# Kernel optimization log

Hardware: AMD Instinct MI355X
Metric: run time of the kernel (lower is better)

The kernel has to match this reference:

```python
import jax, jax.numpy as jnp
import numpy as np

DT_MIN, DT_MAX = 1e-3, 1e-1
LN_EPS = 1e-5


def layernorm(x, w, b):
    mu = jnp.mean(x, axis=-1, keepdims=True)
    var = jnp.mean(jnp.square(x - mu), axis=-1, keepdims=True)
    return (x - mu) * jax.lax.rsqrt(var + LN_EPS) * w + b


def _scan(Lam_bar, Bu, reverse=False):
    # Lam_bar: (P,) complex64; Bu: (B, L, P) complex64
    A = jnp.broadcast_to(Lam_bar, Bu.shape)

    def binop(e_i, e_j):
        a_i, b_i = e_i
        a_j, b_j = e_j
        return a_j * a_i, a_j * b_i + b_j

    _, xs = jax.lax.associative_scan(binop, (A, Bu), axis=1, reverse=reverse)
    return xs  # (B, L, P)


def s5_ssm(u, Lambda_re, Lambda_im, log_step, B_re, B_im, C_re, C_im, D):
    # u: (B, L, H) real. Diagonal S5 with ZOH discretization, bidirectional.
    step = jnp.exp(log_step)                          # (P,)
    Lam = (Lambda_re + 1j * Lambda_im).astype(jnp.complex64)
    Lam_bar = jnp.exp(Lam * step)                     # (P,)
    Bmat = (B_re + 1j * B_im).astype(jnp.complex64)   # (P, H)
    B_bar = ((Lam_bar - 1.0) / Lam)[:, None] * Bmat   # (P, H)
    Bu = jnp.einsum('blh,ph->blp', u.astype(jnp.complex64), B_bar)  # (B,L,P)
    xs_f = _scan(Lam_bar, Bu, reverse=False)
    xs_b = _scan(Lam_bar, Bu, reverse=True)
    xs = jnp.concatenate([xs_f, xs_b], axis=-1)       # (B, L, 2P)
    C = (C_re + 1j * C_im).astype(jnp.complex64)      # (H, 2P)
    ys = 2.0 * jnp.einsum('hp,blp->blh', C, xs).real  # conj-symmetric output
    return ys + D * u


def gelu(x):
    return jax.nn.gelu(x, approximate=False)  # torch default (erf) gelu


def s5_block(x, ln1_w, ln1_b, ln2_w, ln2_b, Lambda_re, Lambda_im, log_step,
             B_re, B_im, C_re, C_im, D, ff_enc_w, ff_dec_w):
    # attention-style half: pre-LN + S5 + gelu + residual (residual = normed input)
    fx = layernorm(x, ln1_w, ln1_b)
    res = fx
    x = gelu(s5_ssm(fx, Lambda_re, Lambda_im, log_step, B_re, B_im, C_re, C_im, D)) + res
    # FFN half: pre-LN + GEGLU + residual (residual = normed input)
    fx = layernorm(x, ln2_w, ln2_b)
    res = fx
    h = fx @ ff_enc_w.T                               # (B, L, 2*dim)
    a, g = jnp.split(h, 2, axis=-1)
    x = (a * gelu(g)) @ ff_dec_w.T + res
    return x


def setup_inputs() -> dict:
    B, L, D_IN, DIM, P = 4, 4096, 512, 1024, 512
    key = jax.random.key(0)
    ks = jax.random.split(key, 16)
    inp = {}
    inp['x'] = jax.random.normal(ks[0], (B, L, D_IN), dtype=jnp.float32)
    inp['W_in'] = jax.random.normal(ks[1], (DIM, D_IN), jnp.float32) / np.sqrt(D_IN)
    inp['W_out'] = jax.random.normal(ks[2], (D_IN, DIM), jnp.float32) / np.sqrt(DIM)
    inp['ln1_w'] = jnp.ones((DIM,), jnp.float32)
    inp['ln1_b'] = jnp.zeros((DIM,), jnp.float32)
    inp['ln2_w'] = jnp.ones((DIM,), jnp.float32)
    inp['ln2_b'] = jnp.zeros((DIM,), jnp.float32)
    inp['Lambda_re'] = -0.5 * jnp.exp(jax.random.normal(ks[3], (P,), jnp.float32))
    inp['Lambda_im'] = jnp.pi * jax.random.normal(ks[4], (P,), jnp.float32)
    inp['log_step'] = jax.random.uniform(ks[5], (P,), jnp.float32,
                                         minval=np.log(DT_MIN), maxval=np.log(DT_MAX))
    inp['B_re'] = jax.random.normal(ks[6], (P, DIM), jnp.float32) / np.sqrt(DIM)
    inp['B_im'] = jax.random.normal(ks[7], (P, DIM), jnp.float32) / np.sqrt(DIM)
    inp['C_re'] = jax.random.normal(ks[8], (DIM, 2 * P), jnp.float32) / np.sqrt(2 * P)
    inp['C_im'] = jax.random.normal(ks[9], (DIM, 2 * P), jnp.float32) / np.sqrt(2 * P)
    inp['D'] = jax.random.normal(ks[10], (DIM,), jnp.float32)
    inp['ff_enc_w'] = jax.random.normal(ks[11], (2 * DIM, DIM), jnp.float32) / np.sqrt(DIM)
    inp['ff_dec_w'] = jax.random.normal(ks[12], (DIM, DIM), jnp.float32) / np.sqrt(DIM)
    return inp


def reference(x, W_in, W_out, ln1_w, ln1_b, ln2_w, ln2_b, Lambda_re, Lambda_im,
              log_step, B_re, B_im, C_re, C_im, D, ff_enc_w, ff_dec_w):
    h = x @ W_in.T                                    # (B, L, dim)
    h = s5_block(h, ln1_w, ln1_b, ln2_w, ln2_b, Lambda_re, Lambda_im, log_step,
                 B_re, B_im, C_re, C_im, D, ff_enc_w, ff_dec_w)
    return h @ W_out.T                                # (B, L, d_input)
```

## Files before the change

kernel.cpp:

```cpp
#include <hip/hip_runtime.h>
#include <cstdint>

typedef __bf16 bf16;
typedef __bf16 bf16x2 __attribute__((ext_vector_type(2)));
typedef __bf16 bf16x4 __attribute__((ext_vector_type(4)));
typedef __bf16 bf16x8 __attribute__((ext_vector_type(8)));
typedef float f32x4 __attribute__((ext_vector_type(4)));

#define MROWS 16384
#define DIMH 1024
#define PDIM 512
#define LSEQ 4096
#define CL 16
#define NC (LSEQ / CL)

typedef const __attribute__((address_space(1))) unsigned int* gas_t;
typedef __attribute__((address_space(3))) unsigned int* las_t;

__device__ __forceinline__ float gelu_f(float x) {
  return 0.5f * x * (1.0f + erff(x * 0.70710678118654752f));
}

__global__ void k_prep(const float* __restrict__ Lre, const float* __restrict__ Lim,
                       const float* __restrict__ lstep,
                       float2* __restrict__ lamb, float2* __restrict__ coef) {
  const int p = blockIdx.x * blockDim.x + threadIdx.x;
  if (p >= PDIM) return;
  const float lre = Lre[p], lim = Lim[p];
  const float st = expf(lstep[p]);
  const float er = expf(lre * st);
  const float lbr = er * cosf(lim * st);
  const float lbi = er * sinf(lim * st);
  lamb[p] = make_float2(lbr, lbi);
  const float ar = lbr - 1.0f, ai = lbi;
  const float d = lre * lre + lim * lim;
  coef[p] = make_float2((ar * lre + ai * lim) / d, (ai * lre - ar * lim) / d);
}

__global__ void k_f32_to_bf16(const float* __restrict__ in, bf16* __restrict__ outp, int n) {
  const int i = (blockIdx.x * 256 + threadIdx.x) * 4;
  if (i >= n) return;
  const float4 v = *(const float4*)(in + i);
  bf16x4 o = { (bf16)v.x, (bf16)v.y, (bf16)v.z, (bf16)v.w };
  *(bf16x4*)(outp + i) = o;
}

__global__ void k_bcat(const float* __restrict__ Bre, const float* __restrict__ Bim,
                       const float2* __restrict__ coef, bf16* __restrict__ bcat) {
  const int idx = blockIdx.x * 256 + threadIdx.x;
  const int p = idx >> 10;
  const float2 c = coef[p];
  const float br = Bre[idx], bi = Bim[idx];
  bcat[idx] = (bf16)(c.x * br - c.y * bi);
  bcat[idx + PDIM * DIMH] = (bf16)(c.x * bi + c.y * br);
}

__global__ void k_ccomb(const float* __restrict__ Cre, const float* __restrict__ Cim,
                        bf16* __restrict__ cc) {
  const int idx = blockIdx.x * 256 + threadIdx.x;
  const int n = idx >> 11, k = idx & 2047;
  float v;
  if (k < 512)       v =  2.0f * Cre[n * 1024 + k];
  else if (k < 1024) v = -2.0f * Cim[n * 1024 + (k - 512)];
  else if (k < 1536) v =  2.0f * Cre[n * 1024 + 512 + (k - 1024)];
  else               v = -2.0f * Cim[n * 1024 + 512 + (k - 1536)];
  cc[idx] = (bf16)v;
}


#define VMCNT4 asm volatile("s_waitcnt vmcnt(4)" ::: "memory")
#define VMCNT0 asm volatile("s_waitcnt vmcnt(0)" ::: "memory")
#define LGKM0  asm volatile("s_waitcnt lgkmcnt(0)" ::: "memory")
#define SCHED0 __builtin_amdgcn_sched_barrier(0)
#define BAR    __builtin_amdgcn_s_barrier()

#define PHASE(slot, kh, mh, LOADB, STAGE_STMT, WAIT_STMT)                      \
  {                                                                            \
    if (LOADB) ldB(slot, kh, bfr);                                             \
    ldA(slot, kh, mh, afr);                                                    \
    STAGE_STMT;                                                                \
    SCHED0;                                                                    \
    BAR;                                                                       \
    LGKM0;                                                                     \
    SCHED0;                                                                    \
    __builtin_amdgcn_s_setprio(1);                                             \
    _Pragma("unroll")                                                          \
    for (int m = 0; m < 4; ++m)                                                \
      _Pragma("unroll")                                                        \
      for (int n = 0; n < 4; ++n)                                              \
        acc[(mh) * 4 + m][n] = __builtin_amdgcn_mfma_f32_16x16x32_bf16(        \
            afr[m], bfr[n], acc[(mh) * 4 + m][n], 0, 0, 0);                    \
    __builtin_amdgcn_s_setprio(0);                                             \
    SCHED0;                                                                    \
    WAIT_STMT;                                                                 \
    BAR;                                                                       \
  }

template <int EPI>
__global__ __launch_bounds__(512, 2) void k_gemm(const bf16* __restrict__ A,
                                                 const bf16* __restrict__ W,
                                                 float* __restrict__ Cf,
                                                 bf16* __restrict__ Cb,
                                                 const bf16* __restrict__ auxb,
                                                 int K, int N, int nbnl) {
  extern __shared__ char lds[];
  const int q = (int)gridDim.x >> 3;
  const int s = ((int)blockIdx.x & 7) * q + ((int)blockIdx.x >> 3);
  const int bm = s >> nbnl;
  const int bn = s & ((1 << nbnl) - 1);
  const int tid = threadIdx.x;
  const int lane = tid & 63;
  const int wave = tid >> 6;
  const int wr = wave >> 2;
  const int wc = wave & 3;

  const size_t arow0 = (size_t)bm * 256;
  const size_t wrow0 = (size_t)bn * 256;
  const int srow = tid >> 2;
  const int schunk = (tid & 3) ^ ((tid >> 3) & 3);
  const int wbase = wave << 10;

  f32x4 acc[8][4];
#pragma unroll
  for (int i = 0; i < 8; ++i)
#pragma unroll
    for (int j = 0; j < 4; ++j) acc[i][j] = (f32x4){0.f, 0.f, 0.f, 0.f};

  auto stage = [&](int slot, int kh, int kt) {
    const int kcol = kt * 64 + kh * 32 + schunk * 8;
    {
      char* base = lds + slot * 32768 + kh * 16384;
      __builtin_amdgcn_global_load_lds(
          (gas_t)(A + (arow0 + srow) * (size_t)K + kcol), (las_t)(base + wbase), 16, 0, 0);
      __builtin_amdgcn_global_load_lds(
          (gas_t)(A + (arow0 + 128 + srow) * (size_t)K + kcol), (las_t)(base + 8192 + wbase), 16, 0, 0);
    }
    {
      char* base = lds + 65536 + slot * 32768 + kh * 16384;
      __builtin_amdgcn_global_load_lds(
          (gas_t)(W + (wrow0 + srow) * (size_t)K + kcol), (las_t)(base + wbase), 16, 0, 0);
      __builtin_amdgcn_global_load_lds(
          (gas_t)(W + (wrow0 + 128 + srow) * (size_t)K + kcol), (las_t)(base + 8192 + wbase), 16, 0, 0);
    }
  };

  auto ldA = [&](int slot, int kh, int mh, bf16x8* af) {
#pragma unroll
    for (int m = 0; m < 4; ++m) {
      const int row = wr * 128 + mh * 64 + m * 16 + (lane & 15);
      const int pc = (lane >> 4) ^ ((row >> 1) & 3);
      af[m] = *(const bf16x8*)(lds + slot * 32768 + kh * 16384 + row * 64 + pc * 16);
    }
  };
  auto ldB = [&](int slot, int kh, bf16x8* bf) {
#pragma unroll
    for (int n = 0; n < 4; ++n) {
      const int row = wc * 64 + n * 16 + (lane & 15);
      const int pc = (lane >> 4) ^ ((row >> 1) & 3);
      bf[n] = *(const bf16x8*)(lds + 65536 + slot * 32768 + kh * 16384 + row * 64 + pc * 16);
    }
  };

  bf16x8 afr[4], bfr[4];

  stage(0, 0, 0);
  stage(0, 1, 0);
  stage(1, 0, 1);
  VMCNT4;
  BAR;

  const int NT = K >> 7;
  for (int t = 0; t < NT; ++t) {
    const int nl = (t + 1 < NT);
    PHASE(0, 0, 0, 1, stage(1, 1, 2 * t + 1), (void)0);
    PHASE(0, 0, 1, 0, (void)0, (void)0);
    PHASE(0, 1, 0, 1, if (nl) stage(0, 0, 2 * t + 2), (void)0);
    if (nl) { PHASE(0, 1, 1, 0, (void)0, VMCNT4); }
    else    { PHASE(0, 1, 1, 0, (void)0, VMCNT0); }
    PHASE(1, 0, 0, 1, if (nl) stage(0, 1, 2 * t + 2), (void)0);
    PHASE(1, 0, 1, 0, (void)0, (void)0);
    PHASE(1, 1, 0, 1, if (nl) stage(1, 0, 2 * t + 3), (void)0);
    if (nl) { PHASE(1, 1, 1, 0, (void)0, VMCNT4); }
    else    { PHASE(1, 1, 1, 0, (void)0, (void)0); }
  }

  const int n0 = (int)wrow0 + wc * 64 + (lane & 15);
  const size_t m0 = arow0 + wr * 128 + ((lane >> 4) << 2);
#pragma unroll
  for (int mi = 0; mi < 8; ++mi)
#pragma unroll
    for (int n = 0; n < 4; ++n) {
      const size_t mb = m0 + mi * 16;
      const int nn = n0 + n * 16;
#pragma unroll
      for (int r = 0; r < 4; ++r) {
        const size_t idx = (mb + r) * (size_t)N + nn;
        const float v = acc[mi][n][r];
        if constexpr (EPI == 0) {
          Cf[idx] = v;
        } else if constexpr (EPI == 1) {
          Cb[idx] = (bf16)((float)auxb[idx] * gelu_f(v));
        } else if constexpr (EPI == 2) {
          Cb[idx] = (bf16)(v + (float)auxb[idx]);
        } else {
          Cb[idx] = (bf16)v;
        }
      }
    }
}

__global__ __launch_bounds__(256) void k_ln(const bf16* __restrict__ X,
                                            const float* __restrict__ w,
                                            const float* __restrict__ bb,
                                            bf16* __restrict__ Yb) {
  const int m = blockIdx.x;
  const int tid = threadIdx.x;
  const bf16x4 v4 = *(const bf16x4*)(X + (size_t)m * DIMH + tid * 4);
  const float v0 = (float)v4[0], v1 = (float)v4[1], v2 = (float)v4[2], v3 = (float)v4[3];
  float s = v0 + v1 + v2 + v3;
  float s2 = v0 * v0 + v1 * v1 + v2 * v2 + v3 * v3;
#pragma unroll
  for (int off = 32; off > 0; off >>= 1) { s += __shfl_down(s, off); s2 += __shfl_down(s2, off); }
  __shared__ float rs[4], rq[4];
  if ((tid & 63) == 0) { rs[tid >> 6] = s; rq[tid >> 6] = s2; }
  __syncthreads();
  s = rs[0] + rs[1] + rs[2] + rs[3];
  s2 = rq[0] + rq[1] + rq[2] + rq[3];
  const float mu = s * (1.0f / DIMH);
  const float inv = rsqrtf(s2 * (1.0f / DIMH) - mu * mu + 1e-5f);
  const float4 wv = ((const float4*)w)[tid];
  const float4 bv = ((const float4*)bb)[tid];
  bf16x4 ob = { (bf16)((v0 - mu) * inv * wv.x + bv.x), (bf16)((v1 - mu) * inv * wv.y + bv.y),
                (bf16)((v2 - mu) * inv * wv.z + bv.z), (bf16)((v3 - mu) * inv * wv.w + bv.w) };
  *(bf16x4*)(Yb + (size_t)m * DIMH + tid * 4) = ob;
}

__global__ __launch_bounds__(256) void k_ln2e(const bf16* __restrict__ YS,
                                              bf16* FXE,
                                              const float* __restrict__ Dv,
                                              const float* __restrict__ w,
                                              const float* __restrict__ bb) {
  const int m = blockIdx.x;
  const int tid = threadIdx.x;
  const bf16x4 ys4 = *(const bf16x4*)(YS + (size_t)m * DIMH + tid * 4);
  const bf16x4 fx4 = *(const bf16x4*)(FXE + (size_t)m * DIMH + tid * 4);
  const float4 dv = ((const float4*)Dv)[tid];
  const float f0 = (float)fx4[0], f1 = (float)fx4[1], f2 = (float)fx4[2], f3 = (float)fx4[3];
  const float t0 = gelu_f((float)ys4[0] + dv.x * f0) + f0;
  const float t1 = gelu_f((float)ys4[1] + dv.y * f1) + f1;
  const float t2 = gelu_f((float)ys4[2] + dv.z * f2) + f2;
  const float t3 = gelu_f((float)ys4[3] + dv.w * f3) + f3;
  float s = t0 + t1 + t2 + t3;
  float s2 = t0 * t0 + t1 * t1 + t2 * t2 + t3 * t3;
#pragma unroll
  for (int off = 32; off > 0; off >>= 1) { s += __shfl_down(s, off); s2 += __shfl_down(s2, off); }
  __shared__ float rs[4], rq[4];
  if ((tid & 63) == 0) { rs[tid >> 6] = s; rq[tid >> 6] = s2; }
  __syncthreads();
  s = rs[0] + rs[1] + rs[2] + rs[3];
  s2 = rq[0] + rq[1] + rq[2] + rq[3];
  const float mu = s * (1.0f / DIMH);
  const float inv = rsqrtf(s2 * (1.0f / DIMH) - mu * mu + 1e-5f);
  const float4 wv = ((const float4*)w)[tid];
  const float4 bv = ((const float4*)bb)[tid];
  bf16x4 ob = { (bf16)((t0 - mu) * inv * wv.x + bv.x), (bf16)((t1 - mu) * inv * wv.y + bv.y),
                (bf16)((t2 - mu) * inv * wv.z + bv.z), (bf16)((t3 - mu) * inv * wv.w + bv.w) };
  *(bf16x4*)(FXE + (size_t)m * DIMH + tid * 4) = ob;
}

__global__ __launch_bounds__(256) void k_scanA(const bf16* __restrict__ Bu,
                                               const float2* __restrict__ lamb,
                                               float2* __restrict__ carry) {
  const int bc = blockIdx.x;
  const int b = bc >> 8, c = bc & (NC - 1);
  const int t = threadIdx.x;
  const size_t rbase = ((size_t)b * LSEQ + (size_t)c * CL) * DIMH;
  float2 re[CL], im[CL];
#pragma unroll
  for (int i = 0; i < CL; ++i) {
    const bf16x2 r2 = *(const bf16x2*)(Bu + rbase + (size_t)i * DIMH + 2 * t);
    const bf16x2 i2 = *(const bf16x2*)(Bu + rbase + (size_t)i * DIMH + PDIM + 2 * t);
    re[i] = make_float2((float)r2[0], (float)r2[1]);
    im[i] = make_float2((float)i2[0], (float)i2[1]);
  }
  const float2 l0 = lamb[2 * t];
  const float2 l1 = lamb[2 * t + 1];
  const size_t cb = ((size_t)bc * 2) * PDIM;
  {
    float s0r = 0.f, s0i = 0.f, s1r = 0.f, s1i = 0.f;
#pragma unroll
    for (int i = 0; i < CL; ++i) {
      float nr = l0.x * s0r - l0.y * s0i + re[i].x;
      float ni = l0.x * s0i + l0.y * s0r + im[i].x;
      s0r = nr; s0i = ni;
      nr = l1.x * s1r - l1.y * s1i + re[i].y;
      ni = l1.x * s1i + l1.y * s1r + im[i].y;
      s1r = nr; s1i = ni;
    }
    carry[cb + 2 * t]     = make_float2(s0r, s0i);
    carry[cb + 2 * t + 1] = make_float2(s1r, s1i);
  }
  {
    float s0r = 0.f, s0i = 0.f, s1r = 0.f, s1i = 0.f;
#pragma unroll
    for (int i = CL - 1; i >= 0; --i) {
      float nr = l0.x * s0r - l0.y * s0i + re[i].x;
      float ni = l0.x * s0i + l0.y * s0r + im[i].x;
      s0r = nr; s0i = ni;
      nr = l1.x * s1r - l1.y * s1i + re[i].y;
      ni = l1.x * s1i + l1.y * s1r + im[i].y;
      s1r = nr; s1i = ni;
    }
    carry[cb + PDIM + 2 * t]     = make_float2(s0r, s0i);
    carry[cb + PDIM + 2 * t + 1] = make_float2(s1r, s1i);
  }
}

__global__ __launch_bounds__(256) void k_scanB(const float2* __restrict__ carry,
                                               const float2* __restrict__ lamb,
                                               float2* __restrict__ seed) {
  const int b = blockIdx.x;
  const int t = threadIdx.x;
  const float2 l0 = lamb[2 * t], l1 = lamb[2 * t + 1];
  float L0r = l0.x, L0i = l0.y, L1r = l1.x, L1i = l1.y;
#pragma unroll
  for (int q = 0; q < 4; ++q) {
    float tr = L0r * L0r - L0i * L0i; L0i = 2.f * L0r * L0i; L0r = tr;
    tr = L1r * L1r - L1i * L1i; L1i = 2.f * L1r * L1i; L1r = tr;
  }
  float S0r = 0.f, S0i = 0.f, S1r = 0.f, S1i = 0.f;
  for (int c = 0; c < NC; ++c) {
    const size_t base = (((size_t)b * NC + c) * 2) * PDIM;
    const float2 c0 = carry[base + 2 * t];
    const float2 c1 = carry[base + 2 * t + 1];
    seed[base + 2 * t]     = make_float2(S0r, S0i);
    seed[base + 2 * t + 1] = make_float2(S1r, S1i);
    float nr = L0r * S0r - L0i * S0i + c0.x;
    float ni = L0r * S0i + L0i * S0r + c0.y;
    S0r = nr; S0i = ni;
    nr = L1r * S1r - L1i * S1i + c1.x;
    ni = L1r * S1i + L1i * S1r + c1.y;
    S1r = nr; S1i = ni;
  }
  S0r = 0.f; S0i = 0.f; S1r = 0.f; S1i = 0.f;
  for (int c = NC - 1; c >= 0; --c) {
    const size_t base = (((size_t)b * NC + c) * 2) * PDIM + PDIM;
    const float2 c0 = carry[base + 2 * t];
    const float2 c1 = carry[base + 2 * t + 1];
    seed[base + 2 * t]     = make_float2(S0r, S0i);
    seed[base + 2 * t + 1] = make_float2(S1r, S1i);
    float nr = L0r * S0r - L0i * S0i + c0.x;
    float ni = L0r * S0i + L0i * S0r + c0.y;
    S0r = nr; S0i = ni;
    nr = L1r * S1r - L1i * S1i + c1.x;
    ni = L1r * S1i + L1i * S1r + c1.y;
    S1r = nr; S1i = ni;
  }
}

__global__ __launch_bounds__(256) void k_scanC(const bf16* __restrict__ Bu,
                                               const float2* __restrict__ lamb,
                                               const float2* __restrict__ seed,
                                               bf16* __restrict__ xs) {
  const int bc = blockIdx.x;
  const int b = bc >> 8, c = bc & (NC - 1);
  const int t = threadIdx.x;
  const size_t rbase = ((size_t)b * LSEQ + (size_t)c * CL) * DIMH;
  float2 re[CL], im[CL];
#pragma unroll
  for (int i = 0; i < CL; ++i) {
    const bf16x2 r2 = *(const bf16x2*)(Bu + rbase + (size_t)i * DIMH + 2 * t);
    const bf16x2 i2 = *(const bf16x2*)(Bu + rbase + (size_t)i * DIMH + PDIM + 2 * t);
    re[i] = make_float2((float)r2[0], (float)r2[1]);
    im[i] = make_float2((float)i2[0], (float)i2[1]);
  }
  const float2 l0 = lamb[2 * t];
  const float2 l1 = lamb[2 * t + 1];
  const size_t sb = ((size_t)bc * 2) * PDIM;
  const size_t obase = ((size_t)b * LSEQ + (size_t)c * CL) * 2048;
  {
    const float2 s0 = seed[sb + 2 * t];
    const float2 s1 = seed[sb + 2 * t + 1];
    float s0r = s0.x, s0i = s0.y, s1r = s1.x, s1i = s1.y;
#pragma unroll
    for (int i = 0; i < CL; ++i) {
      float nr = l0.x * s0r - l0.y * s0i + re[i].x;
      float ni = l0.x * s0i + l0.y * s0r + im[i].x;
      s0r = nr; s0i = ni;
      nr = l1.x * s1r - l1.y * s1i + re[i].y;
      ni = l1.x * s1i + l1.y * s1r + im[i].y;
      s1r = nr; s1i = ni;
      bf16x2 wr2 = { (bf16)s0r, (bf16)s1r };
      bf16x2 wi2 = { (bf16)s0i, (bf16)s1i };
      *(bf16x2*)(xs + obase + (size_t)i * 2048 + 2 * t) = wr2;
      *(bf16x2*)(xs + obase + (size_t)i * 2048 + PDIM + 2 * t) = wi2;
    }
  }
  {
    const float2 s0 = seed[sb + PDIM + 2 * t];
    const float2 s1 = seed[sb + PDIM + 2 * t + 1];
    float s0r = s0.x, s0i = s0.y, s1r = s1.x, s1i = s1.y;
#pragma unroll
    for (int i = CL - 1; i >= 0; --i) {
      float nr = l0.x * s0r - l0.y * s0i + re[i].x;
      float ni = l0.x * s0i + l0.y * s0r + im[i].x;
      s0r = nr; s0i = ni;
      nr = l1.x * s1r - l1.y * s1i + re[i].y;
      ni = l1.x * s1i + l1.y * s1r + im[i].y;
      s1r = nr; s1i = ni;
      bf16x2 wr2 = { (bf16)s0r, (bf16)s1r };
      bf16x2 wi2 = { (bf16)s0i, (bf16)s1i };
      *(bf16x2*)(xs + obase + (size_t)i * 2048 + 1024 + 2 * t) = wr2;
      *(bf16x2*)(xs + obase + (size_t)i * 2048 + 1536 + 2 * t) = wi2;
    }
  }
}

extern "C" void kernel_launch(void* const* d_in, const int* in_sizes, int n_in,
                              void* d_out, int out_size, void* d_ws, size_t ws_size,
                              hipStream_t stream) {
  const float* x    = (const float*)d_in[0];
  const float* W_in = (const float*)d_in[1];
  const float* W_out= (const float*)d_in[2];
  const float* ln1w = (const float*)d_in[3];
  const float* ln1b = (const float*)d_in[4];
  const float* ln2w = (const float*)d_in[5];
  const float* ln2b = (const float*)d_in[6];
  const float* Lre  = (const float*)d_in[7];
  const float* Lim  = (const float*)d_in[8];
  const float* lstep= (const float*)d_in[9];
  const float* Bre  = (const float*)d_in[10];
  const float* Bim  = (const float*)d_in[11];
  const float* Cre  = (const float*)d_in[12];
  const float* Cim  = (const float*)d_in[13];
  const float* Dv   = (const float*)d_in[14];
  const float* ffe  = (const float*)d_in[15];
  const float* ffd  = (const float*)d_in[16];
  float* out = (float*)d_out;
  char* ws = (char*)d_ws;

  bf16* winb   = (bf16*)(ws);
  bf16* woutb  = (bf16*)(ws + (1u << 20));
  bf16* bcat   = (bf16*)(ws + (2u << 20));
  bf16* ccomb  = (bf16*)(ws + (4u << 20));
  bf16* ffeb   = (bf16*)(ws + (8u << 20));
  bf16* ffdb   = (bf16*)(ws + (12u << 20));
  float2* lamb = (float2*)(ws + (14u << 20));
  float2* coef = (float2*)(ws + (14u << 20) + 8192);
  bf16* E      = (bf16*)(ws + (16u << 20));
  bf16* hb     = (bf16*)(ws + (48u << 20));
  bf16* Bub    = (bf16*)(ws + (48u << 20));
  bf16* ysb    = (bf16*)(ws + (48u << 20));
  bf16* x3b    = (bf16*)(ws + (48u << 20));
  bf16* xsb    = (bf16*)(ws + (80u << 20));
  bf16* a_b    = (bf16*)(ws + (80u << 20));
  bf16* G      = (bf16*)(ws + (112u << 20));
  float2* carry = (float2*)(ws + (144u << 20));
  float2* seed  = (float2*)(ws + (152u << 20));

  static bool attr_done = false;
  if (!attr_done) {
    hipFuncSetAttribute((const void*)&k_gemm<0>, hipFuncAttributeMaxDynamicSharedMemorySize, 131072);
    hipFuncSetAttribute((const void*)&k_gemm<1>, hipFuncAttributeMaxDynamicSharedMemorySize, 131072);
    hipFuncSetAttribute((const void*)&k_gemm<2>, hipFuncAttributeMaxDynamicSharedMemorySize, 131072);
    hipFuncSetAttribute((const void*)&k_gemm<3>, hipFuncAttributeMaxDynamicSharedMemorySize, 131072);
    attr_done = true;
  }

  k_prep<<<2, 256, 0, stream>>>(Lre, Lim, lstep, lamb, coef);
  k_f32_to_bf16<<<512, 256, 0, stream>>>(W_in, winb, 524288);
  k_f32_to_bf16<<<512, 256, 0, stream>>>(W_out, woutb, 524288);
  k_f32_to_bf16<<<2048, 256, 0, stream>>>(ffe, ffeb, 2097152);
  k_f32_to_bf16<<<1024, 256, 0, stream>>>(ffd, ffdb, 1048576);
  k_f32_to_bf16<<<8192, 256, 0, stream>>>(x, E, 8388608);
  k_bcat<<<2048, 256, 0, stream>>>(Bre, Bim, coef, bcat);
  k_ccomb<<<8192, 256, 0, stream>>>(Cre, Cim, ccomb);

  k_gemm<3><<<256, 512, 131072, stream>>>(E, winb, nullptr, hb, nullptr, 512, 1024, 2);
  k_ln<<<16384, 256, 0, stream>>>(hb, ln1w, ln1b, E);
  k_gemm<3><<<256, 512, 131072, stream>>>(E, bcat, nullptr, Bub, nullptr, 1024, 1024, 2);
  k_scanA<<<4 * NC, 256, 0, stream>>>(Bub, lamb, carry);
  k_scanB<<<4, 256, 0, stream>>>(carry, lamb, seed);
  k_scanC<<<4 * NC, 256, 0, stream>>>(Bub, lamb, seed, xsb);
  k_gemm<3><<<256, 512, 131072, stream>>>(xsb, ccomb, nullptr, ysb, nullptr, 2048, 1024, 2);
  k_ln2e<<<16384, 256, 0, stream>>>(ysb, E, Dv, ln2w, ln2b);
  k_gemm<3><<<256, 512, 131072, stream>>>(E, ffeb, nullptr, a_b, nullptr, 1024, 1024, 2);
  k_gemm<1><<<256, 512, 131072, stream>>>(E, ffeb + (size_t)1024 * 1024, nullptr, G, a_b, 1024, 1024, 2);
  k_gemm<2><<<256, 512, 131072, stream>>>(G, ffdb, nullptr, x3b, E, 1024, 1024, 2);
  k_gemm<0><<<128, 512, 131072, stream>>>(x3b, woutb, out, nullptr, nullptr, 1024, 512, 1);
}
```

Measured before the change: 477.0 us.

## Double-buffer LDS fragment registers and overlap ds_reads with MFMA in GEMM

Result: slower. 526.4 us (+10.4%).

```diff
diff --git a/kernel.cpp b/kernel.cpp
--- a/kernel.cpp
+++ b/kernel.cpp
@@ -70,31 +70,28 @@
 
 #define VMCNT4 asm volatile("s_waitcnt vmcnt(4)" ::: "memory")
 #define VMCNT0 asm volatile("s_waitcnt vmcnt(0)" ::: "memory")
-#define LGKM0  asm volatile("s_waitcnt lgkmcnt(0)" ::: "memory")
+#define LGKM(N) asm volatile("s_waitcnt lgkmcnt(" #N ")" ::: "memory")
 #define SCHED0 __builtin_amdgcn_sched_barrier(0)
 #define BAR    __builtin_amdgcn_s_barrier()
 
-#define PHASE(slot, kh, mh, LOADB, STAGE_STMT, WAIT_STMT)                      \
-  {                                                                            \
-    if (LOADB) ldB(slot, kh, bfr);                                             \
-    ldA(slot, kh, mh, afr);                                                    \
-    STAGE_STMT;                                                                \
-    SCHED0;                                                                    \
-    BAR;                                                                       \
-    LGKM0;                                                                     \
-    SCHED0;                                                                    \
-    __builtin_amdgcn_s_setprio(1);                                             \
-    _Pragma("unroll")                                                          \
-    for (int m = 0; m < 4; ++m)                                                \
-      _Pragma("unroll")                                                        \
-      for (int n = 0; n < 4; ++n)                                              \
-        acc[(mh) * 4 + m][n] = __builtin_amdgcn_mfma_f32_16x16x32_bf16(        \
-            afr[m], bfr[n], acc[(mh) * 4 + m][n], 0, 0, 0);                    \
-    __builtin_amdgcn_s_setprio(0);                                             \
-    SCHED0;                                                                    \
-    WAIT_STMT;                                                                 \
-    BAR;                                                                       \
-  }
+#define DSREAD(dst, addr, imm) \
+  asm volatile("ds_read_b128 %0, %1 offset:%c2" : "=&v"(dst) : "v"(addr), "i"(imm))
+
+#define ISSUE_A(DST, MH, SLOT, KH)                                   \
+  { _Pragma("unroll") for (int m_ = 0; m_ < 4; ++m_)                 \
+      DSREAD(DST[m_], aA[MH][m_], (SLOT) * 32768 + (KH) * 16384); }
+
+#define ISSUE_B(DST, SLOT, KH)                                       \
+  { _Pragma("unroll") for (int n_ = 0; n_ < 4; ++n_)                 \
+      DSREAD(DST[n_], aB[n_], (SLOT) * 32768 + (KH) * 16384); }
+
+#define MFMA16(ASET, BSET, MH)                                                  \
+  __builtin_amdgcn_s_setprio(1);                                                \
+  _Pragma("unroll") for (int m_ = 0; m_ < 4; ++m_)                              \
+    _Pragma("unroll") for (int n_ = 0; n_ < 4; ++n_)                            \
+      acc[(MH) * 4 + m_][n_] = __builtin_amdgcn_mfma_f32_16x16x32_bf16(         \
+          ASET[m_], BSET[n_], acc[(MH) * 4 + m_][n_], 0, 0, 0);                 \
+  __builtin_amdgcn_s_setprio(0)
 
 template <int EPI>
 __global__ __launch_bounds__(512, 2) void k_gemm(const bf16* __restrict__ A,
@@ -126,6 +123,22 @@
 #pragma unroll
     for (int j = 0; j < 4; ++j) acc[i][j] = (f32x4){0.f, 0.f, 0.f, 0.f};
 
+  uint32_t aA[2][4], aB[4];
+#pragma unroll
+  for (int mh = 0; mh < 2; ++mh)
+#pragma unroll
+    for (int m = 0; m < 4; ++m) {
+      const int row = wr * 128 + mh * 64 + m * 16 + (lane & 15);
+      const int pc = (lane >> 4) ^ ((row >> 1) & 3);
+      aA[mh][m] = (uint32_t)(uintptr_t)(lds + row * 64 + pc * 16);
+    }
+#pragma unroll
+  for (int n = 0; n < 4; ++n) {
+    const int row = wc * 64 + n * 16 + (lane & 15);
+    const int pc = (lane >> 4) ^ ((row >> 1) & 3);
+    aB[n] = (uint32_t)(uintptr_t)(lds + 65536 + row * 64 + pc * 16);
+  }
+
   auto stage = [&](int slot, int kh, int kt) {
     const int kcol = kt * 64 + kh * 32 + schunk * 8;
     {
@@ -144,24 +157,7 @@
     }
   };
 
-  auto ldA = [&](int slot, int kh, int mh, bf16x8* af) {
-#pragma unroll
-    for (int m = 0; m < 4; ++m) {
-      const int row = wr * 128 + mh * 64 + m * 16 + (lane & 15);
-      const int pc = (lane >> 4) ^ ((row >> 1) & 3);
-      af[m] = *(const bf16x8*)(lds + slot * 32768 + kh * 16384 + row * 64 + pc * 16);
-    }
-  };
-  auto ldB = [&](int slot, int kh, bf16x8* bf) {
-#pragma unroll
-    for (int n = 0; n < 4; ++n) {
-      const int row = wc * 64 + n * 16 + (lane & 15);
-      const int pc = (lane >> 4) ^ ((row >> 1) & 3);
-      bf[n] = *(const bf16x8*)(lds + 65536 + slot * 32768 + kh * 16384 + row * 64 + pc * 16);
-    }
-  };
-
-  bf16x8 afr[4], bfr[4];
+  bf16x8 afX[4], afY[4], bfX[4], bfY[4];
 
   stage(0, 0, 0);
   stage(0, 1, 0);
@@ -172,16 +168,50 @@
   const int NT = K >> 7;
   for (int t = 0; t < NT; ++t) {
     const int nl = (t + 1 < NT);
-    PHASE(0, 0, 0, 1, stage(1, 1, 2 * t + 1), (void)0);
-    PHASE(0, 0, 1, 0, (void)0, (void)0);
-    PHASE(0, 1, 0, 1, if (nl) stage(0, 0, 2 * t + 2), (void)0);
-    if (nl) { PHASE(0, 1, 1, 0, (void)0, VMCNT4); }
-    else    { PHASE(0, 1, 1, 0, (void)0, VMCNT0); }
-    PHASE(1, 0, 0, 1, if (nl) stage(0, 1, 2 * t + 2), (void)0);
-    PHASE(1, 0, 1, 0, (void)0, (void)0);
-    PHASE(1, 1, 0, 1, if (nl) stage(1, 0, 2 * t + 3), (void)0);
-    if (nl) { PHASE(1, 1, 1, 0, (void)0, VMCNT4); }
-    else    { PHASE(1, 1, 1, 0, (void)0, (void)0); }
+    ISSUE_A(afX, 0, 0, 0);
+    ISSUE_B(bfX, 0, 0);
+    ISSUE_A(afY, 1, 0, 0);
+    stage(1, 1, 2 * t + 1);
+    LGKM(4); SCHED0;
+    MFMA16(afX, bfX, 0);
+    SCHED0; BAR;
+    ISSUE_A(afX, 0, 0, 1);
+    ISSUE_B(bfY, 0, 1);
+    LGKM(8); SCHED0;
+    MFMA16(afY, bfX, 1);
+    SCHED0; BAR;
+    ISSUE_A(afY, 1, 0, 1);
+    if (nl) stage(0, 0, 2 * t + 2);
+    LGKM(4); SCHED0;
+    MFMA16(afX, bfY, 0);
+    SCHED0; BAR;
+    LGKM(0); SCHED0;
+    MFMA16(afY, bfY, 1);
+    SCHED0;
+    if (nl) { VMCNT4; } else { VMCNT0; }
+    BAR;
+    ISSUE_A(afX, 0, 1, 0);
+    ISSUE_B(bfX, 1, 0);
+    ISSUE_A(afY, 1, 1, 0);
+    if (nl) stage(0, 1, 2 * t + 2);
+    LGKM(4); SCHED0;
+    MFMA16(afX, bfX, 0);
+    SCHED0; BAR;
+    ISSUE_A(afX, 0, 1, 1);
+    ISSUE_B(bfY, 1, 1);
+    LGKM(8); SCHED0;
+    MFMA16(afY, bfX, 1);
+    SCHED0; BAR;
+    ISSUE_A(afY, 1, 1, 1);
+    if (nl) stage(1, 0, 2 * t + 3);
+    LGKM(4); SCHED0;
+    MFMA16(afX, bfY, 0);
+    SCHED0; BAR;
+    LGKM(0); SCHED0;
+    MFMA16(afY, bfY, 1);
+    SCHED0;
+    if (nl) { VMCNT4; }
+    BAR;
   }
 
   const int n0 = (int)wrow0 + wc * 64 + (lane & 15);
```

## Shrink GEMM tiles to 128x128 with 4 waves and fuse prep kernels

Applied to the files above, without the earlier changes.

Result: faster. 449.5 us (-5.8%).

```diff
diff --git a/kernel.cpp b/kernel.cpp
--- a/kernel.cpp
+++ b/kernel.cpp
@@ -21,50 +21,75 @@
   return 0.5f * x * (1.0f + erff(x * 0.70710678118654752f));
 }
 
-__global__ void k_prep(const float* __restrict__ Lre, const float* __restrict__ Lim,
-                       const float* __restrict__ lstep,
-                       float2* __restrict__ lamb, float2* __restrict__ coef) {
-  const int p = blockIdx.x * blockDim.x + threadIdx.x;
-  if (p >= PDIM) return;
-  const float lre = Lre[p], lim = Lim[p];
-  const float st = expf(lstep[p]);
-  const float er = expf(lre * st);
-  const float lbr = er * cosf(lim * st);
-  const float lbi = er * sinf(lim * st);
-  lamb[p] = make_float2(lbr, lbi);
-  const float ar = lbr - 1.0f, ai = lbi;
-  const float d = lre * lre + lim * lim;
-  coef[p] = make_float2((ar * lre + ai * lim) / d, (ai * lre - ar * lim) / d);
-}
-
-__global__ void k_f32_to_bf16(const float* __restrict__ in, bf16* __restrict__ outp, int n) {
-  const int i = (blockIdx.x * 256 + threadIdx.x) * 4;
-  if (i >= n) return;
-  const float4 v = *(const float4*)(in + i);
-  bf16x4 o = { (bf16)v.x, (bf16)v.y, (bf16)v.z, (bf16)v.w };
-  *(bf16x4*)(outp + i) = o;
-}
-
-__global__ void k_bcat(const float* __restrict__ Bre, const float* __restrict__ Bim,
-                       const float2* __restrict__ coef, bf16* __restrict__ bcat) {
-  const int idx = blockIdx.x * 256 + threadIdx.x;
-  const int p = idx >> 10;
-  const float2 c = coef[p];
-  const float br = Bre[idx], bi = Bim[idx];
-  bcat[idx] = (bf16)(c.x * br - c.y * bi);
-  bcat[idx + PDIM * DIMH] = (bf16)(c.x * bi + c.y * br);
-}
-
-__global__ void k_ccomb(const float* __restrict__ Cre, const float* __restrict__ Cim,
-                        bf16* __restrict__ cc) {
-  const int idx = blockIdx.x * 256 + threadIdx.x;
-  const int n = idx >> 11, k = idx & 2047;
-  float v;
-  if (k < 512)       v =  2.0f * Cre[n * 1024 + k];
-  else if (k < 1024) v = -2.0f * Cim[n * 1024 + (k - 512)];
-  else if (k < 1536) v =  2.0f * Cre[n * 1024 + 512 + (k - 1024)];
-  else               v = -2.0f * Cim[n * 1024 + 512 + (k - 1536)];
-  cc[idx] = (bf16)v;
+__global__ __launch_bounds__(256) void k_mega(
+    const float* __restrict__ x, const float* __restrict__ W_in,
+    const float* __restrict__ W_out, const float* __restrict__ ffe,
+    const float* __restrict__ ffd, const float* __restrict__ Lre,
+    const float* __restrict__ Lim, const float* __restrict__ lstep,
+    const float* __restrict__ Bre, const float* __restrict__ Bim,
+    const float* __restrict__ Cre, const float* __restrict__ Cim,
+    bf16* __restrict__ xb, bf16* __restrict__ winb, bf16* __restrict__ woutb,
+    bf16* __restrict__ ffeb, bf16* __restrict__ ffdb, bf16* __restrict__ bcat,
+    bf16* __restrict__ cc, float2* __restrict__ lamb) {
+  const int bid = blockIdx.x;
+  const int tid = threadIdx.x;
+  auto cvt4 = [&](const float* src, bf16* dst, int i4) {
+    const float4 v = *(const float4*)(src + i4);
+    bf16x4 o = { (bf16)v.x, (bf16)v.y, (bf16)v.z, (bf16)v.w };
+    *(bf16x4*)(dst + i4) = o;
+  };
+  if (bid < 8192) {
+    cvt4(x, xb, bid * 1024 + tid * 4);
+  } else if (bid < 8704) {
+    cvt4(W_in, winb, (bid - 8192) * 1024 + tid * 4);
+  } else if (bid < 9216) {
+    cvt4(W_out, woutb, (bid - 8704) * 1024 + tid * 4);
+  } else if (bid < 11264) {
+    cvt4(ffe, ffeb, (bid - 9216) * 1024 + tid * 4);
+  } else if (bid < 12288) {
+    cvt4(ffd, ffdb, (bid - 11264) * 1024 + tid * 4);
+  } else if (bid < 12800) {
+    const int i4 = (bid - 12288) * 1024 + tid * 4;
+    const int p = i4 >> 10;
+    const float lre = Lre[p], lim = Lim[p];
+    const float st = expf(lstep[p]);
+    const float er = expf(lre * st);
+    const float lbr = er * cosf(lim * st);
+    const float lbi = er * sinf(lim * st);
+    const float ar = lbr - 1.0f, ai = lbi;
+    const float d = lre * lre + lim * lim;
+    const float cx = (ar * lre + ai * lim) / d;
+    const float cy = (ai * lre - ar * lim) / d;
+    const float4 br = *(const float4*)(Bre + i4);
+    const float4 bi = *(const float4*)(Bim + i4);
+    bf16x4 o1 = { (bf16)(cx * br.x - cy * bi.x), (bf16)(cx * br.y - cy * bi.y),
+                  (bf16)(cx * br.z - cy * bi.z), (bf16)(cx * br.w - cy * bi.w) };
+    bf16x4 o2 = { (bf16)(cx * bi.x + cy * br.x), (bf16)(cx * bi.y + cy * br.y),
+                  (bf16)(cx * bi.z + cy * br.z), (bf16)(cx * bi.w + cy * br.w) };
+    *(bf16x4*)(bcat + i4) = o1;
+    *(bf16x4*)(bcat + i4 + PDIM * DIMH) = o2;
+  } else if (bid < 14848) {
+    const int i4 = (bid - 12800) * 1024 + tid * 4;
+    const int n = i4 >> 11, k0 = i4 & 2047;
+    const float* src;
+    float sgn;
+    int kk;
+    if (k0 < 512)       { src = Cre + n * 1024;       sgn =  2.0f; kk = k0; }
+    else if (k0 < 1024) { src = Cim + n * 1024;       sgn = -2.0f; kk = k0 - 512; }
+    else if (k0 < 1536) { src = Cre + n * 1024 + 512; sgn =  2.0f; kk = k0 - 1024; }
+    else                { src = Cim + n * 1024 + 512; sgn = -2.0f; kk = k0 - 1536; }
+    const float4 v = *(const float4*)(src + kk);
+    bf16x4 o = { (bf16)(sgn * v.x), (bf16)(sgn * v.y), (bf16)(sgn * v.z), (bf16)(sgn * v.w) };
+    *(bf16x4*)(cc + i4) = o;
+  } else {
+    const int p = (bid - 14848) * 256 + tid;
+    if (p < PDIM) {
+      const float lre = Lre[p], lim = Lim[p];
+      const float st = expf(lstep[p]);
+      const float er = expf(lre * st);
+      lamb[p] = make_float2(er * cosf(lim * st), er * sinf(lim * st));
+    }
+  }
 }
 
 
@@ -74,10 +99,10 @@
 #define SCHED0 __builtin_amdgcn_sched_barrier(0)
 #define BAR    __builtin_amdgcn_s_barrier()
 
-#define PHASE(slot, kh, mh, LOADB, STAGE_STMT, WAIT_STMT)                      \
+#define PHASE(slot, kh, STAGE_STMT, WAIT_STMT)                                 \
   {                                                                            \
-    if (LOADB) ldB(slot, kh, bfr);                                             \
-    ldA(slot, kh, mh, afr);                                                    \
+    ldB(slot, kh, bfr);                                                        \
+    ldA(slot, kh, afr);                                                        \
     STAGE_STMT;                                                                \
     SCHED0;                                                                    \
     BAR;                                                                       \
@@ -88,8 +113,8 @@
     for (int m = 0; m < 4; ++m)                                                \
       _Pragma("unroll")                                                        \
       for (int n = 0; n < 4; ++n)                                              \
-        acc[(mh) * 4 + m][n] = __builtin_amdgcn_mfma_f32_16x16x32_bf16(        \
-            afr[m], bfr[n], acc[(mh) * 4 + m][n], 0, 0, 0);                    \
+        acc[m][n] = __builtin_amdgcn_mfma_f32_16x16x32_bf16(                   \
+            afr[m], bfr[n], acc[m][n], 0, 0, 0);                               \
     __builtin_amdgcn_s_setprio(0);                                             \
     SCHED0;                                                                    \
     WAIT_STMT;                                                                 \
@@ -97,7 +122,7 @@
   }
 
 template <int EPI>
-__global__ __launch_bounds__(512, 2) void k_gemm(const bf16* __restrict__ A,
+__global__ __launch_bounds__(256, 2) void k_gemm(const bf16* __restrict__ A,
                                                  const bf16* __restrict__ W,
                                                  float* __restrict__ Cf,
                                                  bf16* __restrict__ Cb,
@@ -111,45 +136,45 @@
   const int tid = threadIdx.x;
   const int lane = tid & 63;
   const int wave = tid >> 6;
-  const int wr = wave >> 2;
-  const int wc = wave & 3;
-
-  const size_t arow0 = (size_t)bm * 256;
-  const size_t wrow0 = (size_t)bn * 256;
+  const int wr = wave >> 1;
+  const int wc = wave & 1;
+
+  const size_t arow0 = (size_t)bm * 128;
+  const size_t wrow0 = (size_t)bn * 128;
   const int srow = tid >> 2;
   const int schunk = (tid & 3) ^ ((tid >> 3) & 3);
   const int wbase = wave << 10;
 
-  f32x4 acc[8][4];
-#pragma unroll
-  for (int i = 0; i < 8; ++i)
+  f32x4 acc[4][4];
+#pragma unroll
+  for (int i = 0; i < 4; ++i)
 #pragma unroll
     for (int j = 0; j < 4; ++j) acc[i][j] = (f32x4){0.f, 0.f, 0.f, 0.f};
 
   auto stage = [&](int slot, int kh, int kt) {
     const int kcol = kt * 64 + kh * 32 + schunk * 8;
     {
-      char* base = lds + slot * 32768 + kh * 16384;
+      char* base = lds + slot * 16384 + kh * 8192;
       __builtin_amdgcn_global_load_lds(
           (gas_t)(A + (arow0 + srow) * (size_t)K + kcol), (las_t)(base + wbase), 16, 0, 0);
       __builtin_amdgcn_global_load_lds(
-          (gas_t)(A + (arow0 + 128 + srow) * (size_t)K + kcol), (las_t)(base + 8192 + wbase), 16, 0, 0);
+          (gas_t)(A + (arow0 + 64 + srow) * (size_t)K + kcol), (las_t)(base + 4096 + wbase), 16, 0, 0);
     }
     {
-      char* base = lds + 65536 + slot * 32768 + kh * 16384;
+      char* base = lds + 32768 + slot * 16384 + kh * 8192;
       __builtin_amdgcn_global_load_lds(
           (gas_t)(W + (wrow0 + srow) * (size_t)K + kcol), (las_t)(base + wbase), 16, 0, 0);
       __builtin_amdgcn_global_load_lds(
-          (gas_t)(W + (wrow0 + 128 + srow) * (size_t)K + kcol), (las_t)(base + 8192 + wbase), 16, 0, 0);
+          (gas_t)(W + (wrow0 + 64 + srow) * (size_t)K + kcol), (las_t)(base + 4096 + wbase), 16, 0, 0);
     }
   };
 
-  auto ldA = [&](int slot, int kh, int mh, bf16x8* af) {
+  auto ldA = [&](int slot, int kh, bf16x8* af) {
 #pragma unroll
     for (int m = 0; m < 4; ++m) {
-      const int row = wr * 128 + mh * 64 + m * 16 + (lane & 15);
+      const int row = wr * 64 + m * 16 + (lane & 15);
       const int pc = (lane >> 4) ^ ((row >> 1) & 3);
-      af[m] = *(const bf16x8*)(lds + slot * 32768 + kh * 16384 + row * 64 + pc * 16);
+      af[m] = *(const bf16x8*)(lds + slot * 16384 + kh * 8192 + row * 64 + pc * 16);
     }
   };
   auto ldB = [&](int slot, int kh, bf16x8* bf) {
@@ -157,7 +182,7 @@
     for (int n = 0; n < 4; ++n) {
       const int row = wc * 64 + n * 16 + (lane & 15);
       const int pc = (lane >> 4) ^ ((row >> 1) & 3);
-      bf[n] = *(const bf16x8*)(lds + 65536 + slot * 32768 + kh * 16384 + row * 64 + pc * 16);
+      bf[n] = *(const bf16x8*)(lds + 32768 + slot * 16384 + kh * 8192 + row * 64 + pc * 16);
     }
   };
 
@@ -172,22 +197,18 @@
   const int NT = K >> 7;
   for (int t = 0; t < NT; ++t) {
     const int nl = (t + 1 < NT);
-    PHASE(0, 0, 0, 1, stage(1, 1, 2 * t + 1), (void)0);
-    PHASE(0, 0, 1, 0, (void)0, (void)0);
-    PHASE(0, 1, 0, 1, if (nl) stage(0, 0, 2 * t + 2), (void)0);
-    if (nl) { PHASE(0, 1, 1, 0, (void)0, VMCNT4); }
-    else    { PHASE(0, 1, 1, 0, (void)0, VMCNT0); }
-    PHASE(1, 0, 0, 1, if (nl) stage(0, 1, 2 * t + 2), (void)0);
-    PHASE(1, 0, 1, 0, (void)0, (void)0);
-    PHASE(1, 1, 0, 1, if (nl) stage(1, 0, 2 * t + 3), (void)0);
-    if (nl) { PHASE(1, 1, 1, 0, (void)0, VMCNT4); }
-    else    { PHASE(1, 1, 1, 0, (void)0, (void)0); }
+    PHASE(0, 0, stage(1, 1, 2 * t + 1), (void)0);
+    if (nl) { PHASE(0, 1, stage(0, 0, 2 * t + 2), VMCNT4); }
+    else    { PHASE(0, 1, (void)0, VMCNT0); }
+    PHASE(1, 0, if (nl) stage(0, 1, 2 * t + 2), (void)0);
+    if (nl) { PHASE(1, 1, stage(1, 0, 2 * t + 3), VMCNT4); }
+    else    { PHASE(1, 1, (void)0, (void)0); }
   }
 
   const int n0 = (int)wrow0 + wc * 64 + (lane & 15);
-  const size_t m0 = arow0 + wr * 128 + ((lane >> 4) << 2);
-#pragma unroll
-  for (int mi = 0; mi < 8; ++mi)
+  const size_t m0 = arow0 + wr * 64 + ((lane >> 4) << 2);
+#pragma unroll
+  for (int mi = 0; mi < 4; ++mi)
 #pragma unroll
     for (int n = 0; n < 4; ++n) {
       const size_t mb = m0 + mi * 16;
@@ -446,7 +467,6 @@
   bf16* ffeb   = (bf16*)(ws + (8u << 20));
   bf16* ffdb   = (bf16*)(ws + (12u << 20));
   float2* lamb = (float2*)(ws + (14u << 20));
-  float2* coef = (float2*)(ws + (14u << 20) + 8192);
   bf16* E      = (bf16*)(ws + (16u << 20));
   bf16* hb     = (bf16*)(ws + (48u << 20));
   bf16* Bub    = (bf16*)(ws + (48u << 20));
@@ -460,32 +480,27 @@
 
   static bool attr_done = false;
   if (!attr_done) {
-    hipFuncSetAttribute((const void*)&k_gemm<0>, hipFuncAttributeMaxDynamicSharedMemorySize, 131072);
-    hipFuncSetAttribute((const void*)&k_gemm<1>, hipFuncAttributeMaxDynamicSharedMemorySize, 131072);
-    hipFuncSetAttribute((const void*)&k_gemm<2>, hipFuncAttributeMaxDynamicSharedMemorySize, 131072);
-    hipFuncSetAttribute((const void*)&k_gemm<3>, hipFuncAttributeMaxDynamicSharedMemorySize, 131072);
+    hipFuncSetAttribute((const void*)&k_gemm<0>, hipFuncAttributeMaxDynamicSharedMemorySize, 65536);
+    hipFuncSetAttribute((const void*)&k_gemm<1>, hipFuncAttributeMaxDynamicSharedMemorySize, 65536);
+    hipFuncSetAttribute((const void*)&k_gemm<2>, hipFuncAttributeMaxDynamicSharedMemorySize, 65536);
+    hipFuncSetAttribute((const void*)&k_gemm<3>, hipFuncAttributeMaxDynamicSharedMemorySize, 65536);
     attr_done = true;
   }
 
-  k_prep<<<2, 256, 0, stream>>>(Lre, Lim, lstep, lamb, coef);
-  k_f32_to_bf16<<<512, 256, 0, stream>>>(W_in, winb, 524288);
-  k_f32_to_bf16<<<512, 256, 0, stream>>>(W_out, woutb, 524288);
-  k_f32_to_bf16<<<2048, 256, 0, stream>>>(ffe, ffeb, 2097152);
-  k_f32_to_bf16<<<1024, 256, 0, stream>>>(ffd, ffdb, 1048576);
-  k_f32_to_bf16<<<8192, 256, 0, stream>>>(x, E, 8388608);
-  k_bcat<<<2048, 256, 0, stream>>>(Bre, Bim, coef, bcat);
-  k_ccomb<<<8192, 256, 0, stream>>>(Cre, Cim, ccomb);
-
-  k_gemm<3><<<256, 512, 131072, stream>>>(E, winb, nullptr, hb, nullptr, 512, 1024, 2);
+  k_mega<<<14850, 256, 0, stream>>>(x, W_in, W_out, ffe, ffd, Lre, Lim, lstep,
+                                    Bre, Bim, Cre, Cim,
+                                    E, winb, woutb, ffeb, ffdb, bcat, ccomb, lamb);
+
+  k_gemm<3><<<1024, 256, 65536, stream>>>(E, winb, nullptr, hb, nullptr, 512, 1024, 3);
   k_ln<<<16384, 256, 0, stream>>>(hb, ln1w, ln1b, E);
-  k_gemm<3><<<256, 512, 131072, stream>>>(E, bcat, nullptr, Bub, nullptr, 1024, 1024, 2);
+  k_gemm<3><<<1024, 256, 65536, stream>>>(E, bcat, nullptr, Bub, nullptr, 1024, 1024, 3);
   k_scanA<<<4 * NC, 256, 0, stream>>>(Bub, lamb, carry);
   k_scanB<<<4, 256, 0, stream>>>(carry, lamb, seed);
   k_scanC<<<4 * NC, 256, 0, stream>>>(Bub, lamb, seed, xsb);
-  k_gemm<3><<<256, 512, 131072, stream>>>(xsb, ccomb, nullptr, ysb, nullptr, 2048, 1024, 2);
+  k_gemm<3><<<1024, 256, 65536, stream>>>(xsb, ccomb, nullptr, ysb, nullptr, 2048, 1024, 3);
   k_ln2e<<<16384, 256, 0, stream>>>(ysb, E, Dv, ln2w, ln2b);
-  k_gemm<3><<<256, 512, 131072, stream>>>(E, ffeb, nullptr, a_b, nullptr, 1024, 1024, 2);
-  k_gemm<1><<<256, 512, 131072, stream>>>(E, ffeb + (size_t)1024 * 1024, nullptr, G, a_b, 1024, 1024, 2);
-  k_gemm<2><<<256, 512, 131072, stream>>>(G, ffdb, nullptr, x3b, E, 1024, 1024, 2);
-  k_gemm<0><<<128, 512, 131072, stream>>>(x3b, woutb, out, nullptr, nullptr, 1024, 512, 1);
-}
+  k_gemm<3><<<1024, 256, 65536, stream>>>(E, ffeb, nullptr, a_b, nullptr, 1024, 1024, 3);
+  k_gemm<1><<<1024, 256, 65536, stream>>>(E, ffeb + (size_t)1024 * 1024, nullptr, G, a_b, 1024, 1024, 3);
+  k_gemm<2><<<1024, 256, 65536, stream>>>(G, ffdb, nullptr, x3b, E, 1024, 1024, 3);
+  k_gemm<0><<<512, 256, 65536, stream>>>(x3b, woutb, out, nullptr, nullptr, 1024, 512, 2);
+}
```
